# Performance work log

Measured on AMD Instinct MI355X. Metric: run time of the kernel, lower is better.

Reference implementation:

```python
import jax, jax.numpy as jnp
import numpy as np

B = 50000      # batch of graphs
NOBJ = 7       # tangram pieces per graph
HID = 64
EMB = 32
SIGMA = 25.0   # VE-SDE sigma for marginal_prob_std


def _lin_init(k, fin, fout):
    kw, kb = jax.random.split(k)
    s = 1.0 / np.sqrt(fin)
    w = jax.random.uniform(kw, (fin, fout), minval=-s, maxval=s, dtype=jnp.float32)
    b = jax.random.uniform(kb, (fout,), minval=-s, maxval=s, dtype=jnp.float32)
    return w, b


def setup_inputs() -> dict:
    key = jax.random.key(0)
    ks = jax.random.split(key, 16)
    N = B * NOBJ
    omega = jax.random.normal(ks[0], (N, 3), dtype=jnp.float32)
    t = jax.random.uniform(ks[1], (B, 1), minval=1e-3, maxval=1.0, dtype=jnp.float32)
    # fully-connected edges (no self loops) per graph, offset by graph index
    a, b = np.meshgrid(np.arange(NOBJ), np.arange(NOBJ), indexing='ij')
    m = a != b
    src0, dst0 = a[m], b[m]                       # (42,)
    offs = (np.arange(B) * NOBJ)[:, None]         # (B,1)
    src = (src0[None, :] + offs).reshape(-1)
    dst = (dst0[None, :] + offs).reshape(-1)
    edge_index = jnp.asarray(np.stack([src, dst]), dtype=jnp.int32)  # (2, B*42)
    W_fourier = jax.random.normal(ks[2], (EMB // 2,), dtype=jnp.float32) * 30.0
    wi1, bi1 = _lin_init(ks[3], 3, HID)
    wi2, bi2 = _lin_init(ks[4], HID, HID)
    wt, bt = _lin_init(ks[5], EMB, EMB)
    w1a, b1a = _lin_init(ks[6], HID * 2, HID)
    w1b, b1b = _lin_init(ks[7], HID, HID)
    w2a, b2a = _lin_init(ks[8], (HID + EMB) * 2, HID)
    w2b, b2b = _lin_init(ks[9], HID, HID)
    w3a, b3a = _lin_init(ks[10], (HID + EMB) * 2, HID)
    w3b, b3b = _lin_init(ks[11], HID, 3)
    return dict(omega=omega, edge_index=edge_index, t=t, num_objs=NOBJ,
                W_fourier=W_fourier,
                wi1=wi1, bi1=bi1, wi2=wi2, bi2=bi2, wt=wt, bt=bt,
                w1a=w1a, b1a=b1a, w1b=w1b, b1b=b1b,
                w2a=w2a, b2a=b2a, w2b=w2b, b2b=b2b,
                w3a=w3a, b3a=b3a, w3b=w3b, b3b=b3b)


def _mlp(x, wa, ba, wb, bb):
    return jax.nn.relu(x @ wa + ba) @ wb + bb


def reference(omega, edge_index, t, num_objs, W_fourier,
              wi1, bi1, wi2, bi2, wt, bt,
              w1a, b1a, w1b, b1b, w2a, b2a, w2b, b2b, w3a, b3a, w3b, b3b):
    N = omega.shape[0]
    src, dst = edge_index[0], edge_index[1]

    def edge_conv(x, wa, ba, wb, bb):
        # EdgeConv: msg = mlp([x_i, x_j - x_i]); max-aggregate at target i
        xi = x[dst]
        msg = _mlp(jnp.concatenate([xi, x[src] - xi], axis=-1), wa, ba, wb, bb)
        return jax.ops.segment_max(msg, dst, num_segments=N)

    init_feature = _mlp(omega, wi1, bi1, wi2, bi2)          # (N, HID)
    # Gaussian Fourier time embedding -> ReLU -> Linear -> ReLU
    proj = t[:, 0][:, None] * W_fourier[None, :] * (2.0 * jnp.pi)   # (B, EMB/2)
    emb = jnp.concatenate([jnp.sin(proj), jnp.cos(proj)], axis=-1)  # (B, EMB)
    xs = jax.nn.relu(jax.nn.relu(emb) @ wt + bt)                    # (B, EMB)
    # torch: xs.repeat(1, num_objs, 1).view(B*num_objs, -1) == tile whole block
    x_sigma = jnp.tile(xs, (num_objs, 1))                           # (N, EMB)

    x = jax.nn.relu(edge_conv(init_feature, w1a, b1a, w1b, b1b))
    x = jnp.concatenate([x, x_sigma], axis=-1)
    x = jax.nn.relu(edge_conv(x, w2a, b2a, w2b, b2b))
    x = jnp.concatenate([x, x_sigma], axis=-1)
    x = edge_conv(x, w3a, b3a, w3b, b3b)                            # (N, 3)

    # torch: t.repeat(1, num_objs).view(B*num_objs, -1) == repeat_interleave
    t_r = jnp.repeat(t, num_objs, axis=0)                           # (N, 1)
    std = jnp.sqrt((SIGMA ** (2.0 * t_r) - 1.0) / (2.0 * jnp.log(SIGMA)))
    return x / (std + 1e-7)
```

## Files before the change

kernel.cpp:

```cpp
#include <hip/hip_runtime.h>


#define NB 50000

typedef unsigned short u16;
typedef unsigned int u32;
typedef short short8 __attribute__((ext_vector_type(8)));
typedef float f32x4 __attribute__((ext_vector_type(4)));
typedef unsigned int u32x4 __attribute__((ext_vector_type(4)));

#define OFF_I  0
#define OFF_1A 8192
#define OFF_2A 24576
#define OFF_3A 49152
#define OFF_1B 73728
#define OFF_2B 81920
#define OFF_WT 90112
#define OFF_3B 92160

#define XSTR 272
#define PQS  304
#define SOFF 8512
#define SSTR 264
#define WREG 12736

__device__ __forceinline__ float b2f(u16 u) {
    return __uint_as_float(((u32)u) << 16);
}
__device__ __forceinline__ u16 f2b(float f) {
    u32 u = __float_as_uint(f);
    u += 0x7FFFu + ((u >> 16) & 1u);
    return (u16)(u >> 16);
}
__device__ __forceinline__ void split2(float v, u16& h, u16& l) {
    u32 u = __float_as_uint(v);
    h = (u16)(u >> 16);
    float d = v - __uint_as_float(u & 0xffff0000u);
    l = f2b(d);
}
__device__ __forceinline__ u32 splitpack(float v) {
    u32 u = __float_as_uint(v);
    float d = v - __uint_as_float(u & 0xffff0000u);
    u32 r = __float_as_uint(d);
    r += 0x7FFFu + ((r >> 16) & 1u);
    return __builtin_amdgcn_perm(r, u, 0x07060302);
}
__device__ __forceinline__ float bcast(float v, int l) {
    return __uint_as_float(__builtin_amdgcn_readlane(__float_as_uint(v), l));
}

__global__ __launch_bounds__(128) void pack_kernel(
    const float* __restrict__ wi2, const float* __restrict__ w1a,
    const float* __restrict__ w2a, const float* __restrict__ w3a,
    const float* __restrict__ w1b, const float* __restrict__ w2b,
    const float* __restrict__ wt,  const float* __restrict__ w3b,
    u16* __restrict__ ws)
{
    int blk = blockIdx.x;
    int j    = blockIdx.y;
    int half = threadIdx.x >> 6;
    int lane = threadIdx.x & 63;
    float v;
    u16* dst;
    if (blk < 88) {
        const float* src; int NT, qoff, obase, frag;
        if (blk < 8)       { src = wi2; NT = 4; qoff = 0;  obase = OFF_I;  frag = blk;      }
        else if (blk < 24) { src = w1a; NT = 8; qoff = 64; obase = OFF_1A; frag = blk - 8;  }
        else if (blk < 48) { src = w2a; NT = 8; qoff = 96; obase = OFF_2A; frag = blk - 24; }
        else if (blk < 72) { src = w3a; NT = 8; qoff = 96; obase = OFF_3A; frag = blk - 48; }
        else if (blk < 80) { src = w1b; NT = 4; qoff = 0;  obase = OFF_1B; frag = blk - 72; }
        else               { src = w2b; NT = 4; qoff = 0;  obase = OFF_2B; frag = blk - 80; }
        int kt = frag / NT, nt = frag % NT;
        int k = kt * 32 + (lane >> 4) * 8 + j;
        int n = nt * 16 + (lane & 15);
        int idx = (n < 64) ? (k * 64 + n) : ((qoff + k) * 64 + (n - 64));
        v = src[idx];
        dst = ws + obase + frag * 1024 + half * 512 + lane * 8 + j;
    } else if (blk < 90) {
        int frag = blk - 88;
        int k = (lane >> 4) * 8 + j;
        int n = frag * 16 + (lane & 15);
        v = wt[k * 32 + n];
        dst = ws + OFF_WT + frag * 1024 + half * 512 + lane * 8 + j;
    } else {
        int frag = blk - 90;
        int k = frag * 32 + (lane >> 4) * 8 + j;
        int n = lane & 15;
        v = (n < 3) ? w3b[k * 3 + n] : 0.f;
        dst = ws + OFF_3B + frag * 1024 + half * 512 + lane * 8 + j;
    }
    u16 hi = f2b(v);
    *dst = (half == 0) ? hi : f2b(v - b2f(hi));
}

__device__ __forceinline__ f32x4 mfma1(short8 a, short8 b, f32x4 acc) {
    return __builtin_amdgcn_mfma_f32_16x16x32_bf16(a, b, acc, 0, 0, 0);
}
__device__ __forceinline__ f32x4 mfma3(short8 ah, short8 al, short8 bh, short8 bl, f32x4 acc) {
    acc = mfma1(ah, bh, acc);
    acc = mfma1(ah, bl, acc);
    acc = mfma1(al, bh, acc);
    return acc;
}

#define ROW(k) ((k) < 7 ? (k) : (k) + 1)

__device__ __forceinline__ void putX(char* G, int k, int L, float v) {
    *(u32*)(G + ROW(k) * XSTR + L * 4) = splitpack(v);
}
__device__ __forceinline__ void unpack8(const uint4& a0, const uint4& a1,
                                        short8& Ah, short8& Al) {
    u32 h0 = __builtin_amdgcn_perm(a0.y, a0.x, 0x05040100);
    u32 h1 = __builtin_amdgcn_perm(a0.w, a0.z, 0x05040100);
    u32 h2 = __builtin_amdgcn_perm(a1.y, a1.x, 0x05040100);
    u32 h3 = __builtin_amdgcn_perm(a1.w, a1.z, 0x05040100);
    u32 l0 = __builtin_amdgcn_perm(a0.y, a0.x, 0x07060302);
    u32 l1 = __builtin_amdgcn_perm(a0.w, a0.z, 0x07060302);
    u32 l2 = __builtin_amdgcn_perm(a1.y, a1.x, 0x07060302);
    u32 l3 = __builtin_amdgcn_perm(a1.w, a1.z, 0x07060302);
    u32x4 hv = {h0, h1, h2, h3}, lv = {l0, l1, l2, l3};
    Ah = __builtin_bit_cast(short8, hv);
    Al = __builtin_bit_cast(short8, lv);
}
__device__ __forceinline__ void loadA2(const char* G, int L, short8* Ah, short8* Al) {
#pragma unroll
    for (int kt = 0; kt < 2; ++kt) {
        const char* base = G + (L & 15) * XSTR + kt * 128 + (L >> 4) * 32;
        uint4 a0 = *(const uint4*)(base);
        uint4 a1 = *(const uint4*)(base + 16);
        unpack8(a0, a1, Ah[kt], Al[kt]);
    }
}
template<int KT, int NT>
__device__ __forceinline__ void lin_pass(const u16* __restrict__ ws, int off, int nt0,
                                         const short8* Ah, const short8* Al,
                                         char* Sg, int L) {
#pragma unroll
    for (int ntc = 0; ntc < 4; ++ntc) {
        f32x4 a1 = {0.f, 0.f, 0.f, 0.f}, a2 = {0.f, 0.f, 0.f, 0.f};
#pragma unroll
        for (int kt = 0; kt < KT; ++kt) {
            int f = kt * NT + nt0 + ntc;
            short8 bh = *(const short8*)(ws + off + f * 1024 + L * 8);
            short8 bl = *(const short8*)(ws + off + f * 1024 + 512 + L * 8);
            a1 = mfma1(Ah[kt], bh, a1);
            a2 = mfma1(Ah[kt], bl, a2);
            a2 = mfma1(Al[kt], bh, a2);
        }
#pragma unroll
        for (int rr = 0; rr < 4; ++rr)
            *(float*)(Sg + ((L >> 4) * 4 + rr) * SSTR + ntc * 64 + (L & 15) * 4) = a1[rr] + a2[rr];
    }
}
__device__ __forceinline__ void copyQ(char* PQ, const char* Sb, int L) {
#pragma unroll
    for (int k = 0; k < 14; ++k)
        *(float*)(PQ + (14 + k) * PQS + L * 4) =
            *(const float*)(Sb + ROW(k) * SSTR + L * 4);
}
__device__ __forceinline__ void fixP(char* PQ, const char* Sb, float vb, int L) {
#pragma unroll
    for (int k = 0; k < 14; ++k) {
        float p = *(const float*)(Sb + ROW(k) * SSTR + L * 4);
        float q = *(const float*)(PQ + (14 + k) * PQS + L * 4);
        *(float*)(PQ + k * PQS + L * 4) = p + vb - q;
    }
}
__device__ __forceinline__ void pack2(float a, float b, u32& H, u32& Lo) {
    u32 ua = __float_as_uint(a), ub = __float_as_uint(b);
    H = __builtin_amdgcn_perm(ub, ua, 0x07060302);
    float da = a - __uint_as_float(ua & 0xffff0000u);
    float db = b - __uint_as_float(ub & 0xffff0000u);
    u32 r;
    asm("v_cvt_pk_bf16_f32 %0, %1, %2" : "=v"(r) : "v"(da), "v"(db));
    Lo = r;
}
__device__ __forceinline__ void buildA1(const char* bp, const char* bq,
                                        short8& Ah, short8& Al) {
    f32x4 p0 = *(const f32x4*)bp,  p1 = *(const f32x4*)(bp + 16);
    f32x4 q0 = *(const f32x4*)bq,  q1 = *(const f32x4*)(bq + 16);
    float h0 = fmaxf(p0[0] + q0[0], 0.f), h1 = fmaxf(p0[1] + q0[1], 0.f);
    float h2 = fmaxf(p0[2] + q0[2], 0.f), h3 = fmaxf(p0[3] + q0[3], 0.f);
    float h4 = fmaxf(p1[0] + q1[0], 0.f), h5 = fmaxf(p1[1] + q1[1], 0.f);
    float h6 = fmaxf(p1[2] + q1[2], 0.f), h7 = fmaxf(p1[3] + q1[3], 0.f);
    u32 H0, H1, H2, H3, L0, L1, L2, L3;
    pack2(h0, h1, H0, L0);
    pack2(h2, h3, H1, L1);
    pack2(h4, h5, H2, L2);
    pack2(h6, h7, H3, L3);
    u32x4 Hv = {H0, H1, H2, H3};
    u32x4 Lv = {L0, L1, L2, L3};
    Ah = __builtin_bit_cast(short8, Hv);
    Al = __builtin_bit_cast(short8, Lv);
}
__device__ __forceinline__ void buildA(const char* PQ, int c, int L,
                                       short8& Ah0, short8& Al0,
                                       short8& Ah1, short8& Al1) {
    int e  = c * 16 + (L & 15);
    int gb = (e >= 42) ? 1 : 0;
    int el = e - gb * 42;
    int i  = el / 6;
    int jj = el - i * 6;
    int j  = jj + (jj >= i);
    const char* bp = PQ + (gb * 7 + i) * PQS + (L >> 4) * 32;
    const char* bq = PQ + (14 + gb * 7 + j) * PQS + (L >> 4) * 32;
    buildA1(bp,       bq,       Ah0, Al0);
    buildA1(bp + 128, bq + 128, Ah1, Al1);
}
__device__ __forceinline__ void maxread(const char* Sb, int cc, float* mx, int L) {
#pragma unroll
    for (int r = 0; r < 16; ++r) {
        int e = cc * 16 + r;
        if (e < 84) {
            int gb = (e >= 42) ? 1 : 0;
            int i = (e - gb * 42) / 6;
            float sv = *(const float*)(Sb + r * SSTR + L * 4);
            mx[gb * 7 + i] = fmaxf(mx[gb * 7 + i], sv);
        }
    }
}

__device__ __forceinline__ void edgeconv_pipe(const u16* __restrict__ ws, int offB,
                                              char* W, char* Sb, float vb, int L) {
    const char* PQ = W;
    float mx[14];
#pragma unroll
    for (int k = 0; k < 14; ++k) mx[k] = -3.0e38f;
    short8 Ah0, Ah1, Al0, Al1;
    buildA(PQ, 0, L, Ah0, Al0, Ah1, Al1);
#pragma unroll
    for (int c = 0; c < 6; ++c) {
        if (c > 0) maxread(Sb, c - 1, mx, L);
#pragma unroll
        for (int nt = 0; nt < 4; ++nt) {
            short8 bh0 = *(const short8*)(ws + offB + nt * 1024 + L * 8);
            short8 bl0 = *(const short8*)(ws + offB + nt * 1024 + 512 + L * 8);
            short8 bh1 = *(const short8*)(ws + offB + (4 + nt) * 1024 + L * 8);
            short8 bl1 = *(const short8*)(ws + offB + (4 + nt) * 1024 + 512 + L * 8);
            f32x4 a1 = {0.f, 0.f, 0.f, 0.f}, a2 = {0.f, 0.f, 0.f, 0.f};
            a1 = mfma1(Ah0, bh0, a1);
            a2 = mfma1(Ah0, bl0, a2);
            a2 = mfma1(Al0, bh0, a2);
            a1 = mfma1(Ah1, bh1, a1);
            a2 = mfma1(Ah1, bl1, a2);
            a2 = mfma1(Al1, bh1, a2);
#pragma unroll
            for (int rr = 0; rr < 4; ++rr)
                *(float*)(Sb + ((L >> 4) * 4 + rr) * SSTR + nt * 64 + (L & 15) * 4) = a1[rr] + a2[rr];
        }
        if (c < 5) buildA(PQ, c + 1, L, Ah0, Al0, Ah1, Al1);
    }
    maxread(Sb, 5, mx, L);
#pragma unroll
    for (int k = 0; k < 14; ++k)
        putX(W, k, L, fmaxf(mx[k] + vb, 0.f));
}

__global__ __launch_bounds__(128, 3) void gnn_kernel(
    const float* __restrict__ omega, const float* __restrict__ tt, const float* __restrict__ Wf,
    const float* __restrict__ wi1, const float* __restrict__ bi1, const float* __restrict__ bi2,
    const float* __restrict__ bt,
    const float* __restrict__ b1a, const float* __restrict__ b1b,
    const float* __restrict__ b2a, const float* __restrict__ b2b,
    const float* __restrict__ b3a, const float* __restrict__ b3b,
    const u16* __restrict__ ws, float* __restrict__ out)
{
    __shared__ __align__(16) char smem[2 * WREG];
    const int L   = threadIdx.x & 63;
    const int wav = threadIdx.x >> 6;
    const int p   = blockIdx.x * 2 + wav;
    const int g0  = p * 2;
    const int base0 = g0 * 7;
    char* W   = smem + wav * WREG;
    char* Sb  = W + SOFF;

    float omv = (L < 42) ? omega[base0 * 3 + L] : 0.f;
    float vwi10 = wi1[L], vwi11 = wi1[64 + L], vwi12 = wi1[128 + L];
    float vbi1 = bi1[L];

    short8 Ah2, Al2;
    {
        int cc = L & 31;
        float vwf = Wf[cc & 15] * 6.283185307179586f;
        int tb = base0 - (base0 / NB) * NB;
#pragma unroll
        for (int k = 0; k < 14; ++k) {
            int ti = tb + k; if (ti >= NB) ti -= NB;
            float pj = tt[ti] * vwf;
            float remb = fmaxf((cc < 16) ? __sinf(pj) : __cosf(pj), 0.f);
            u16 h, l;
            split2(remb, h, l);
            if (L < 32) *(u16*)(W + ROW(k) * XSTR + cc * 4) = h;
            else *(u16*)(W + ROW(k) * XSTR + cc * 4 + 2) = l;
        }
        short8 Eh, El;
        {
            const char* base = W + (L & 15) * XSTR + (L >> 4) * 32;
            uint4 a0 = *(const uint4*)(base);
            uint4 a1 = *(const uint4*)(base + 16);
            unpack8(a0, a1, Eh, El);
        }
#pragma unroll
        for (int nt = 0; nt < 2; ++nt) {
            short8 bh = *(const short8*)(ws + OFF_WT + nt * 1024 + L * 8);
            short8 bl = *(const short8*)(ws + OFF_WT + nt * 1024 + 512 + L * 8);
            f32x4 acc = {0.f, 0.f, 0.f, 0.f};
            acc = mfma3(Eh, El, bh, bl, acc);
#pragma unroll
            for (int rr = 0; rr < 4; ++rr)
                *(float*)(Sb + ((L >> 4) * 4 + rr) * SSTR + nt * 64 + (L & 15) * 4) = acc[rr];
        }
        float vbt = bt[cc];
#pragma unroll
        for (int k = 0; k < 14; ++k) {
            float xv = fmaxf(*(const float*)(Sb + ROW(k) * SSTR + cc * 4) + vbt, 0.f);
            u16 h, l;
            split2(xv, h, l);
            if (L < 32) *(u16*)(W + ROW(k) * XSTR + cc * 4) = h;
            else *(u16*)(W + ROW(k) * XSTR + cc * 4 + 2) = l;
        }
        const char* base = W + (L & 15) * XSTR + (L >> 4) * 32;
        uint4 a0 = *(const uint4*)(base);
        uint4 a1 = *(const uint4*)(base + 16);
        unpack8(a0, a1, Ah2, Al2);
    }

    short8 Ah[3], Al[3];

#pragma unroll
    for (int k = 0; k < 14; ++k) {
        float a0 = bcast(omv, 3 * k), a1 = bcast(omv, 3 * k + 1), a2 = bcast(omv, 3 * k + 2);
        putX(W, k, L, fmaxf(fmaf(a0, vwi10, fmaf(a1, vwi11, fmaf(a2, vwi12, vbi1))), 0.f));
    }

    loadA2(W, L, Ah, Al);
    lin_pass<2, 4>(ws, OFF_I, 0, Ah, Al, Sb, L);
    {
        float vbi2 = bi2[L];
#pragma unroll
        for (int k = 0; k < 14; ++k)
            putX(W, k, L, *(const float*)(Sb + ROW(k) * SSTR + L * 4) + vbi2);
    }

    loadA2(W, L, Ah, Al);
    lin_pass<2, 8>(ws, OFF_1A, 4, Ah, Al, Sb, L);
    copyQ(W, Sb, L);
    lin_pass<2, 8>(ws, OFF_1A, 0, Ah, Al, Sb, L);
    fixP(W, Sb, b1a[L], L);
    edgeconv_pipe(ws, OFF_1B, W, Sb, b1b[L], L);

    loadA2(W, L, Ah, Al);
    Ah[2] = Ah2; Al[2] = Al2;
    lin_pass<3, 8>(ws, OFF_2A, 4, Ah, Al, Sb, L);
    copyQ(W, Sb, L);
    lin_pass<3, 8>(ws, OFF_2A, 0, Ah, Al, Sb, L);
    fixP(W, Sb, b2a[L], L);
    edgeconv_pipe(ws, OFF_2B, W, Sb, b2b[L], L);

    loadA2(W, L, Ah, Al);
    Ah[2] = Ah2; Al[2] = Al2;
    lin_pass<3, 8>(ws, OFF_3A, 4, Ah, Al, Sb, L);
    copyQ(W, Sb, L);
    lin_pass<3, 8>(ws, OFF_3A, 0, Ah, Al, Sb, L);
    fixP(W, Sb, b3a[L], L);

    {
        const char* PQ = W;
        short8 B0h = *(const short8*)(ws + OFF_3B + L * 8);
        short8 B0l = *(const short8*)(ws + OFF_3B + 512 + L * 8);
        short8 B1h = *(const short8*)(ws + OFF_3B + 1024 + L * 8);
        short8 B1l = *(const short8*)(ws + OFF_3B + 1536 + L * 8);
        short8 Ah0, Ah1, Al0, Al1;
        buildA(PQ, 0, L, Ah0, Al0, Ah1, Al1);
#pragma unroll
        for (int c = 0; c < 6; ++c) {
            f32x4 a1 = {0.f, 0.f, 0.f, 0.f}, a2 = {0.f, 0.f, 0.f, 0.f};
            a1 = mfma1(Ah0, B0h, a1);
            a2 = mfma1(Ah0, B0l, a2);
            a2 = mfma1(Al0, B0h, a2);
            a1 = mfma1(Ah1, B1h, a1);
            a2 = mfma1(Ah1, B1l, a2);
            a2 = mfma1(Al1, B1h, a2);
            if ((L & 15) < 3) {
#pragma unroll
                for (int rr = 0; rr < 4; ++rr)
                    *(float*)(Sb + (c * 16 + (L >> 4) * 4 + rr) * 16 + (L & 15) * 4) = a1[rr] + a2[rr];
            }
            if (c < 5) buildA(PQ, c + 1, L, Ah0, Al0, Ah1, Al1);
        }
        if (L < 42) {
            int gb = (L >= 21) ? 1 : 0;
            int ll = L - gb * 21;
            int i = ll / 3, col = ll - i * 3;
            int e0 = gb * 42 + i * 6;
            float m = -3.0e38f;
#pragma unroll
            for (int e6 = 0; e6 < 6; ++e6)
                m = fmaxf(m, *(const float*)(Sb + (e0 + e6) * 16 + col * 4));
            m += b3b[col];
            float tg = tt[g0 + gb];
            float stdv = sqrtf((exp2f(tg * 9.287712379549448f) - 1.0f) * 0.15533740282828987f);
            out[base0 * 3 + L] = m / (stdv + 1e-7f);
        }
    }
}

extern "C" void kernel_launch(void* const* d_in, const int* in_sizes, int n_in,
                              void* d_out, int out_size, void* d_ws, size_t ws_size,
                              hipStream_t stream) {
    const float* omega = (const float*)d_in[0];
    const float* tt  = (const float*)d_in[2];
    const float* Wf  = (const float*)d_in[4];
    const float* wi1 = (const float*)d_in[5];
    const float* bi1 = (const float*)d_in[6];
    const float* wi2 = (const float*)d_in[7];
    const float* bi2 = (const float*)d_in[8];
    const float* wt  = (const float*)d_in[9];
    const float* bt  = (const float*)d_in[10];
    const float* w1a = (const float*)d_in[11];
    const float* b1a = (const float*)d_in[12];
    const float* w1b = (const float*)d_in[13];
    const float* b1b = (const float*)d_in[14];
    const float* w2a = (const float*)d_in[15];
    const float* b2a = (const float*)d_in[16];
    const float* w2b = (const float*)d_in[17];
    const float* b2b = (const float*)d_in[18];
    const float* w3a = (const float*)d_in[19];
    const float* b3a = (const float*)d_in[20];
    const float* w3b = (const float*)d_in[21];
    const float* b3b = (const float*)d_in[22];
    u16* ws = (u16*)d_ws;

    pack_kernel<<<dim3(92, 8), dim3(128), 0, stream>>>(wi2, w1a, w2a, w3a, w1b, w2b, wt, w3b, ws);
    gnn_kernel<<<dim3(12500), dim3(128), 0, stream>>>(
        omega, tt, Wf, wi1, bi1, bi2, bt,
        b1a, b1b, b2a, b2b, b3a, b3b, ws, (float*)d_out);
}
```

Before: 401.8 us.

## Remap edge rows to padded per-node groups and reduce max in registers

Edges are renumbered so each 16-row MFMA tile holds two nodes with eight padded edge slots each, with duplicate neighbours filling the unused slots. The segment max can then be taken inside the accumulator registers with a swizzle and a bpermute, so the LDS store-and-reread through the scratch buffer goes away. In exchange each edgeconv and the final layer run seven tiles instead of six, about 17% more MFMA work, and the final layer's readback indexing changes to match.

```diff
diff --git a/kernel.cpp b/kernel.cpp
--- a/kernel.cpp
+++ b/kernel.cpp
@@ -47,6 +47,12 @@
 }
 __device__ __forceinline__ float bcast(float v, int l) {
     return __uint_as_float(__builtin_amdgcn_readlane(__float_as_uint(v), l));
+}
+__device__ __forceinline__ float swzx16(float v) {
+    return __uint_as_float(__builtin_amdgcn_ds_swizzle(__float_as_uint(v), 0x401F));
+}
+__device__ __forceinline__ float bpx32(float v, int L) {
+    return __uint_as_float(__builtin_amdgcn_ds_bpermute((L ^ 32) << 2, __float_as_uint(v)));
 }
 
 __global__ __launch_bounds__(128) void pack_kernel(
@@ -196,41 +202,30 @@
 __device__ __forceinline__ void buildA(const char* PQ, int c, int L,
                                        short8& Ah0, short8& Al0,
                                        short8& Ah1, short8& Al1) {
-    int e  = c * 16 + (L & 15);
-    int gb = (e >= 42) ? 1 : 0;
-    int el = e - gb * 42;
-    int i  = el / 6;
-    int jj = el - i * 6;
-    int j  = jj + (jj >= i);
-    const char* bp = PQ + (gb * 7 + i) * PQS + (L >> 4) * 32;
+    int r  = L & 15;
+    int k  = 2 * c + (r >> 3);
+    int s  = r & 7;
+    int gb = (k >= 7) ? 1 : 0;
+    int i  = k - gb * 7;
+    int ss = (s > 5) ? 0 : s;
+    int j  = ss + (ss >= i);
+    const char* bp = PQ + k * PQS + (L >> 4) * 32;
     const char* bq = PQ + (14 + gb * 7 + j) * PQS + (L >> 4) * 32;
     buildA1(bp,       bq,       Ah0, Al0);
     buildA1(bp + 128, bq + 128, Ah1, Al1);
 }
-__device__ __forceinline__ void maxread(const char* Sb, int cc, float* mx, int L) {
-#pragma unroll
-    for (int r = 0; r < 16; ++r) {
-        int e = cc * 16 + r;
-        if (e < 84) {
-            int gb = (e >= 42) ? 1 : 0;
-            int i = (e - gb * 42) / 6;
-            float sv = *(const float*)(Sb + r * SSTR + L * 4);
-            mx[gb * 7 + i] = fmaxf(mx[gb * 7 + i], sv);
-        }
-    }
-}
 
 __device__ __forceinline__ void edgeconv_pipe(const u16* __restrict__ ws, int offB,
-                                              char* W, char* Sb, float vb, int L) {
+                                              char* W, float vb, int L) {
     const char* PQ = W;
+    const int g = L >> 4;
+    const bool lo32 = (L < 32);
     float mx[14];
-#pragma unroll
-    for (int k = 0; k < 14; ++k) mx[k] = -3.0e38f;
     short8 Ah0, Ah1, Al0, Al1;
     buildA(PQ, 0, L, Ah0, Al0, Ah1, Al1);
 #pragma unroll
-    for (int c = 0; c < 6; ++c) {
-        if (c > 0) maxread(Sb, c - 1, mx, L);
+    for (int c = 0; c < 7; ++c) {
+        float mA = 0.f, mB = 0.f;
 #pragma unroll
         for (int nt = 0; nt < 4; ++nt) {
             short8 bh0 = *(const short8*)(ws + offB + nt * 1024 + L * 8);
@@ -244,13 +239,20 @@
             a1 = mfma1(Ah1, bh1, a1);
             a2 = mfma1(Ah1, bl1, a2);
             a2 = mfma1(Al1, bh1, a2);
-#pragma unroll
-            for (int rr = 0; rr < 4; ++rr)
-                *(float*)(Sb + ((L >> 4) * 4 + rr) * SSTR + nt * 64 + (L & 15) * 4) = a1[rr] + a2[rr];
-        }
-        if (c < 5) buildA(PQ, c + 1, L, Ah0, Al0, Ah1, Al1);
-    }
-    maxread(Sb, 5, mx, L);
+            float v0 = a1[0] + a2[0], v1 = a1[1] + a2[1];
+            float v2 = a1[2] + a2[2], v3 = a1[3] + a2[3];
+            float m  = fmaxf(fmaxf(v0, v1), fmaxf(v2, v3));
+            float own = fmaxf(m, swzx16(m));
+            float oth = bpx32(own, L);
+            float a = lo32 ? own : oth;
+            float b = lo32 ? oth : own;
+            if (nt == 0)      { mA = a; mB = b; }
+            else if (g == nt) { mA = a; mB = b; }
+        }
+        mx[2 * c]     = mA;
+        mx[2 * c + 1] = mB;
+        if (c < 6) buildA(PQ, c + 1, L, Ah0, Al0, Ah1, Al1);
+    }
 #pragma unroll
     for (int k = 0; k < 14; ++k)
         putX(W, k, L, fmaxf(mx[k] + vb, 0.f));
@@ -347,7 +349,7 @@
     copyQ(W, Sb, L);
     lin_pass<2, 8>(ws, OFF_1A, 0, Ah, Al, Sb, L);
     fixP(W, Sb, b1a[L], L);
-    edgeconv_pipe(ws, OFF_1B, W, Sb, b1b[L], L);
+    edgeconv_pipe(ws, OFF_1B, W, b1b[L], L);
 
     loadA2(W, L, Ah, Al);
     Ah[2] = Ah2; Al[2] = Al2;
@@ -355,7 +357,7 @@
     copyQ(W, Sb, L);
     lin_pass<3, 8>(ws, OFF_2A, 0, Ah, Al, Sb, L);
     fixP(W, Sb, b2a[L], L);
-    edgeconv_pipe(ws, OFF_2B, W, Sb, b2b[L], L);
+    edgeconv_pipe(ws, OFF_2B, W, b2b[L], L);
 
     loadA2(W, L, Ah, Al);
     Ah[2] = Ah2; Al[2] = Al2;
@@ -373,7 +375,7 @@
         short8 Ah0, Ah1, Al0, Al1;
         buildA(PQ, 0, L, Ah0, Al0, Ah1, Al1);
 #pragma unroll
-        for (int c = 0; c < 6; ++c) {
+        for (int c = 0; c < 7; ++c) {
             f32x4 a1 = {0.f, 0.f, 0.f, 0.f}, a2 = {0.f, 0.f, 0.f, 0.f};
             a1 = mfma1(Ah0, B0h, a1);
             a2 = mfma1(Ah0, B0l, a2);
@@ -386,17 +388,17 @@
                 for (int rr = 0; rr < 4; ++rr)
                     *(float*)(Sb + (c * 16 + (L >> 4) * 4 + rr) * 16 + (L & 15) * 4) = a1[rr] + a2[rr];
             }
-            if (c < 5) buildA(PQ, c + 1, L, Ah0, Al0, Ah1, Al1);
+            if (c < 6) buildA(PQ, c + 1, L, Ah0, Al0, Ah1, Al1);
         }
         if (L < 42) {
             int gb = (L >= 21) ? 1 : 0;
             int ll = L - gb * 21;
             int i = ll / 3, col = ll - i * 3;
-            int e0 = gb * 42 + i * 6;
+            int r0 = (gb * 7 + i) * 8;
             float m = -3.0e38f;
 #pragma unroll
-            for (int e6 = 0; e6 < 6; ++e6)
-                m = fmaxf(m, *(const float*)(Sb + (e0 + e6) * 16 + col * 4));
+            for (int s = 0; s < 6; ++s)
+                m = fmaxf(m, *(const float*)(Sb + (r0 + s) * 16 + col * 4));
             m += b3b[col];
             float tg = tt[g0 + gb];
             float stdv = sqrtf((exp2f(tg * 9.287712379549448f) - 1.0f) * 0.15533740282828987f);
```

Result: slower. 423.5 us (+5.4%).
